# Performance work log

Hardware: AMD Instinct MI355X
Metric: run time of the kernel (lower is better)

## Reference

```python
import jax, jax.numpy as jnp
import numpy as np

DIM = 3            # point feature dim (xyz)
POS_HID = 64       # pos_mlp hidden
ATTN_HID = DIM * 4 # attn_mlp hidden (mult=4)
N_NBR = 16         # points per group
GROUPS = 512       # groups per batch element
MLP_D = N_NBR * DIM  # 48


def setup_inputs() -> dict:
    key = jax.random.key(0)
    ks = jax.random.split(key, 20)
    B = 32
    s = lambda *sh: 1.0 / np.sqrt(sh[0])
    inp = {
        "original_points": jax.random.normal(ks[0], (B, GROUPS, DIM), jnp.float32),
        "data": jax.random.normal(ks[1], (B, GROUPS, N_NBR, DIM), jnp.float32),
        # PointTransformerLayer params
        "w_qkv": jax.random.normal(ks[2], (DIM, DIM * 3), jnp.float32) * s(DIM),
        "pos_w1": jax.random.normal(ks[3], (3, POS_HID), jnp.float32) * s(3),
        "pos_b1": jnp.zeros((POS_HID,), jnp.float32),
        "pos_w2": jax.random.normal(ks[4], (POS_HID, DIM), jnp.float32) * s(POS_HID),
        "pos_b2": jnp.zeros((DIM,), jnp.float32),
        "attn_w1": jax.random.normal(ks[5], (DIM, ATTN_HID), jnp.float32) * s(DIM),
        "attn_b1": jnp.zeros((ATTN_HID,), jnp.float32),
        "attn_w2": jax.random.normal(ks[6], (ATTN_HID, DIM), jnp.float32) * s(ATTN_HID),
        "attn_b2": jnp.zeros((DIM,), jnp.float32),
        # downstream MLP params
        "mlp_w1": jax.random.normal(ks[7], (MLP_D, MLP_D), jnp.float32) * s(MLP_D),
        "mlp_b1": jnp.zeros((MLP_D,), jnp.float32),
        "mlp_w2": jax.random.normal(ks[8], (MLP_D, MLP_D), jnp.float32) * s(MLP_D),
        "mlp_b2": jnp.zeros((MLP_D,), jnp.float32),
        "mlp_w3": jax.random.normal(ks[9], (MLP_D, 1), jnp.float32) * s(MLP_D),
        "mlp_b3": jnp.zeros((1,), jnp.float32),
    }
    return inp


def reference(original_points, data, w_qkv, pos_w1, pos_b1, pos_w2, pos_b2,
              attn_w1, attn_b1, attn_w2, attn_b2,
              mlp_w1, mlp_b1, mlp_w2, mlp_b2, mlp_w3, mlp_b3):
    B, G, n, d = data.shape
    x = data.reshape(B * G, n, d)          # (BG, n, 3)
    pos = x[:, :, :3]                       # pos == features here (f=3)

    # Point-transformer vector attention
    qkv = x @ w_qkv                          # (BG, n, 9)
    q, k, v = jnp.split(qkv, 3, axis=-1)
    rel_pos = pos[:, :, None, :] - pos[:, None, :, :]              # (BG, n, n, 3)
    rel_emb = jax.nn.relu(rel_pos @ pos_w1 + pos_b1) @ pos_w2 + pos_b2  # (BG, n, n, 3)
    qk_rel = q[:, :, None, :] - k[:, None, :, :]                   # (BG, n, n, 3)
    v_ij = v[:, None, :, :] + rel_emb                              # (BG, n, n, 3)
    sim = jax.nn.relu((qk_rel + rel_emb) @ attn_w1 + attn_b1) @ attn_w2 + attn_b2
    attn = jax.nn.softmax(sim, axis=-2)                            # softmax over j
    agg = jnp.einsum('bijd,bijd->bid', attn, v_ij)                 # (BG, n, 3)

    # regroup into (B, 512, 48) exactly as stack(split(512, dim=0))
    sa = agg.reshape(B, G, n * d)
    h = jax.nn.relu(sa @ mlp_w1 + mlp_b1)
    h = jax.nn.relu(h @ mlp_w2 + mlp_b2)
    return h @ mlp_w3 + mlp_b3              # (B, 512, 1)
```

## Files before the change

kernel.cpp:

```cpp
#include <hip/hip_runtime.h>


typedef _Float16 h2 __attribute__((ext_vector_type(2)));
typedef _Float16 h8 __attribute__((ext_vector_type(8)));

#define AH_STRIDE 36
#define WP_STRIDE 36

union H8U { h8 v; h2 p[4]; unsigned u[4]; };

__device__ __forceinline__ h2 pkrtz(float a, float b) {
    return __builtin_bit_cast(h2, __builtin_amdgcn_cvt_pkrtz(a, b));
}

#if __has_builtin(__builtin_amdgcn_fdot2)
__device__ __forceinline__ float dot2acc(h2 a, h2 b, float c) {
    return __builtin_amdgcn_fdot2(a, b, c, false);
}
#else
__device__ __forceinline__ float dot2acc(h2 a, h2 b, float c) {
    return fmaf((float)a.x, (float)b.x, fmaf((float)a.y, (float)b.y, c));
}
#endif

__device__ __forceinline__ float dpp_add16(float x) {
    float s = x;
    int t;
    t = __builtin_amdgcn_update_dpp(0, __builtin_bit_cast(int, s), 0x121, 0xf, 0xf, false);
    s += __builtin_bit_cast(float, t);
    t = __builtin_amdgcn_update_dpp(0, __builtin_bit_cast(int, s), 0x122, 0xf, 0xf, false);
    s += __builtin_bit_cast(float, t);
    t = __builtin_amdgcn_update_dpp(0, __builtin_bit_cast(int, s), 0x124, 0xf, 0xf, false);
    s += __builtin_bit_cast(float, t);
    t = __builtin_amdgcn_update_dpp(0, __builtin_bit_cast(int, s), 0x128, 0xf, 0xf, false);
    s += __builtin_bit_cast(float, t);
    return s;
}

__global__ __launch_bounds__(256) void pt_main(
    const float* __restrict__ data,
    const float* __restrict__ wqkv,
    const float* __restrict__ pw1,
    const float* __restrict__ pb1,
    const float* __restrict__ pw2,
    const float* __restrict__ pb2,
    const float* __restrict__ aw1,
    const float* __restrict__ ab1,
    const float* __restrict__ aw2,
    const float* __restrict__ ab2,
    const float* __restrict__ mw1,
    const float* __restrict__ mb1,
    const float* __restrict__ mw2,
    const float* __restrict__ mb2,
    const float* __restrict__ mw3,
    const float* __restrict__ mb3,
    float* __restrict__ out)
{
    __shared__ __attribute__((aligned(16))) float s_pos[48];
    __shared__ __attribute__((aligned(16))) float s_q[48], s_k[48], s_v[48];
    __shared__ __attribute__((aligned(16))) float s_sa[48], s_h1[48];
    __shared__ __attribute__((aligned(16))) unsigned s_a1h[16 * AH_STRIDE];
    __shared__ __attribute__((aligned(16))) unsigned s_a2h[16 * AH_STRIDE];
    __shared__ __attribute__((aligned(16))) unsigned s_wp[3 * WP_STRIDE];

    const int g = blockIdx.x;
    const int t = threadIdx.x;

    if (t < 48) s_pos[t] = data[g * 48 + t];
    __syncthreads();

    if (t < 48) {
        const int sec = t >> 4, p = t & 15;
        const float x0 = s_pos[p*3+0], x1 = s_pos[p*3+1], x2 = s_pos[p*3+2];
        float* dst = (sec == 0) ? s_q : (sec == 1) ? s_k : s_v;
        #pragma unroll
        for (int c = 0; c < 3; ++c) {
            dst[p*3+c] = fmaf(x0, wqkv[0*9 + sec*3 + c],
                         fmaf(x1, wqkv[1*9 + sec*3 + c],
                         x2 * wqkv[2*9 + sec*3 + c]));
        }
    }

    {
        const int ii = t >> 4;
        const int hc = (t & 15) << 2;
        const float x0 = s_pos[ii*3+0], x1 = s_pos[ii*3+1], x2 = s_pos[ii*3+2];
        float s[4];
        #pragma unroll
        for (int c = 0; c < 4; ++c) {
            const int h = hc + c;
            s[c] = fmaf(x0, pw1[h], fmaf(x1, pw1[64+h], x2 * pw1[128+h]));
        }
        h2 a1p0 = pkrtz(s[0] + pb1[hc+0], s[1] + pb1[hc+1]);
        h2 a1p1 = pkrtz(s[2] + pb1[hc+2], s[3] + pb1[hc+3]);
        h2 a2p0 = pkrtz(s[0], s[1]);
        h2 a2p1 = pkrtz(s[2], s[3]);
        const int base = ii * AH_STRIDE + (hc >> 1);
        s_a1h[base+0] = __builtin_bit_cast(unsigned, a1p0);
        s_a1h[base+1] = __builtin_bit_cast(unsigned, a1p1);
        s_a2h[base+0] = __builtin_bit_cast(unsigned, a2p0);
        s_a2h[base+1] = __builtin_bit_cast(unsigned, a2p1);
    }

    if (t < 96) {
        const int hp = t & 31, c = t >> 5;
        h2 wpair = pkrtz(pw2[(2*hp)*3 + c], pw2[(2*hp+1)*3 + c]);
        s_wp[c * WP_STRIDE + hp] = __builtin_bit_cast(unsigned, wpair);
    }
    __syncthreads();

    const int i = t >> 4, j = t & 15;

    float e0 = pb2[0], e1 = pb2[1], e2 = pb2[2];
    #pragma unroll
    for (int cc = 0; cc < 8; ++cc) {
        H8U ai, aj, w0, w1, w2;
        ai.v = *(const h8*)&s_a1h[i * AH_STRIDE + cc*4];
        aj.v = *(const h8*)&s_a2h[j * AH_STRIDE + cc*4];
        w0.v = *(const h8*)&s_wp[0 * WP_STRIDE + cc*4];
        w1.v = *(const h8*)&s_wp[1 * WP_STRIDE + cc*4];
        w2.v = *(const h8*)&s_wp[2 * WP_STRIDE + cc*4];
        #pragma unroll
        for (int m = 0; m < 4; ++m) {
            h2 d = ai.p[m] - aj.p[m];
            h2 z = {(_Float16)0, (_Float16)0};
            h2 r = { d.x > z.x ? d.x : z.x, d.y > z.y ? d.y : z.y };
            e0 = dot2acc(r, w0.p[m], e0);
            e1 = dot2acc(r, w1.p[m], e1);
            e2 = dot2acc(r, w2.p[m], e2);
        }
    }

    const float vi0 = s_v[j*3+0] + e0, vi1 = s_v[j*3+1] + e1, vi2 = s_v[j*3+2] + e2;
    const float si0 = s_q[i*3+0] - s_k[j*3+0] + e0;
    const float si1 = s_q[i*3+1] - s_k[j*3+1] + e1;
    const float si2 = s_q[i*3+2] - s_k[j*3+2] + e2;

    float m0 = ab2[0], m1 = ab2[1], m2 = ab2[2];
    #pragma unroll
    for (int gg = 0; gg < 12; ++gg) {
        float hg = fmaf(si0, aw1[gg], fmaf(si1, aw1[12+gg], fmaf(si2, aw1[24+gg], ab1[gg])));
        hg = fmaxf(hg, 0.0f);
        m0 = fmaf(hg, aw2[gg*3+0], m0);
        m1 = fmaf(hg, aw2[gg*3+1], m1);
        m2 = fmaf(hg, aw2[gg*3+2], m2);
    }

    const float L2E = 1.44269504f;
    const float p0 = __builtin_amdgcn_exp2f(m0 * L2E);
    const float p1 = __builtin_amdgcn_exp2f(m1 * L2E);
    const float p2 = __builtin_amdgcn_exp2f(m2 * L2E);

    const float n0 = dpp_add16(p0 * vi0);
    const float n1 = dpp_add16(p1 * vi1);
    const float n2 = dpp_add16(p2 * vi2);
    const float d0 = dpp_add16(p0);
    const float d1 = dpp_add16(p1);
    const float d2 = dpp_add16(p2);

    if (j == 0) {
        s_sa[i*3+0] = n0 * __builtin_amdgcn_rcpf(d0);
        s_sa[i*3+1] = n1 * __builtin_amdgcn_rcpf(d1);
        s_sa[i*3+2] = n2 * __builtin_amdgcn_rcpf(d2);
    }
    __syncthreads();

    if (t < 48) {
        float h1 = mb1[t];
        #pragma unroll
        for (int c = 0; c < 48; ++c) h1 = fmaf(s_sa[c], mw1[c*48+t], h1);
        s_h1[t] = fmaxf(h1, 0.0f);
    }
    __syncthreads();

    float fv = 0.0f;
    if (t < 48) {
        float h2v = mb2[t];
        #pragma unroll
        for (int c = 0; c < 48; ++c) h2v = fmaf(s_h1[c], mw2[c*48+t], h2v);
        h2v = fmaxf(h2v, 0.0f);
        fv = h2v * mw3[t];
    }
    if (t < 64) {
        #pragma unroll
        for (int mk = 1; mk < 64; mk <<= 1) fv += __shfl_xor(fv, mk);
        if (t == 0) out[g] = fv + mb3[0];
    }
}

extern "C" void kernel_launch(void* const* d_in, const int* in_sizes, int n_in,
                              void* d_out, int out_size, void* d_ws, size_t ws_size,
                              hipStream_t stream) {
    const float* data = (const float*)d_in[1];
    const int groups = out_size;

    pt_main<<<groups, 256, 0, stream>>>(
        data,
        (const float*)d_in[2],  (const float*)d_in[3],  (const float*)d_in[4],
        (const float*)d_in[5],  (const float*)d_in[6],  (const float*)d_in[7],
        (const float*)d_in[8],  (const float*)d_in[9],  (const float*)d_in[10],
        (const float*)d_in[11], (const float*)d_in[12], (const float*)d_in[13],
        (const float*)d_in[14], (const float*)d_in[15], (const float*)d_in[16],
        (float*)d_out);
}
```

Before: 143.6 us.

## Prepack fp16 weights in a pre-kernel and run attention MLP in packed half

Adds a tiny pre-kernel that packs the pos_mlp second-layer and attn_mlp weights and biases into fp16 pairs in the workspace. The main kernel then reads them as uniform (scalar) loads instead of building them in shared memory per block. The attn_mlp hidden layer is recomputed with packed half FMAs and dot2 accumulation. q/k/v are stored padded to float4 so each needs a single vector LDS load. This adds a second launch and lowers precision in the attention MLP, which risks accuracy.

```diff
diff --git a/kernel.cpp b/kernel.cpp
--- a/kernel.cpp
+++ b/kernel.cpp
@@ -5,12 +5,14 @@
 typedef _Float16 h8 __attribute__((ext_vector_type(8)));
 
 #define AH_STRIDE 36
-#define WP_STRIDE 36
 
 union H8U { h8 v; h2 p[4]; unsigned u[4]; };
 
 __device__ __forceinline__ h2 pkrtz(float a, float b) {
     return __builtin_bit_cast(h2, __builtin_amdgcn_cvt_pkrtz(a, b));
+}
+__device__ __forceinline__ h2 uash2(unsigned u) {
+    return __builtin_bit_cast(h2, u);
 }
 
 #if __has_builtin(__builtin_amdgcn_fdot2)
@@ -35,6 +37,25 @@
     t = __builtin_amdgcn_update_dpp(0, __builtin_bit_cast(int, s), 0x128, 0xf, 0xf, false);
     s += __builtin_bit_cast(float, t);
     return s;
+}
+
+__global__ void wpack(const float* __restrict__ pw2, const float* __restrict__ aw1,
+                      const float* __restrict__ ab1, const float* __restrict__ aw2,
+                      unsigned* __restrict__ ws) {
+    const int t = threadIdx.x;
+    if (t < 96) {
+        const int hp = t & 31, c = t >> 5;
+        ws[c*32+hp] = __builtin_bit_cast(unsigned, pkrtz(pw2[(2*hp)*3+c], pw2[(2*hp+1)*3+c]));
+    } else if (t < 114) {
+        const int idx = t - 96, r = idx / 6, gp = idx % 6;
+        ws[96+r*6+gp] = __builtin_bit_cast(unsigned, pkrtz(aw1[r*12+2*gp], aw1[r*12+2*gp+1]));
+    } else if (t < 120) {
+        const int gp = t - 114;
+        ws[114+gp] = __builtin_bit_cast(unsigned, pkrtz(ab1[2*gp], ab1[2*gp+1]));
+    } else if (t < 138) {
+        const int idx = t - 120, gp = idx / 3, c = idx % 3;
+        ws[120+gp*3+c] = __builtin_bit_cast(unsigned, pkrtz(aw2[(2*gp)*3+c], aw2[(2*gp+1)*3+c]));
+    }
 }
 
 __global__ __launch_bounds__(256) void pt_main(
@@ -42,11 +63,7 @@
     const float* __restrict__ wqkv,
     const float* __restrict__ pw1,
     const float* __restrict__ pb1,
-    const float* __restrict__ pw2,
     const float* __restrict__ pb2,
-    const float* __restrict__ aw1,
-    const float* __restrict__ ab1,
-    const float* __restrict__ aw2,
     const float* __restrict__ ab2,
     const float* __restrict__ mw1,
     const float* __restrict__ mb1,
@@ -54,14 +71,14 @@
     const float* __restrict__ mb2,
     const float* __restrict__ mw3,
     const float* __restrict__ mb3,
+    const unsigned* __restrict__ wsp,
     float* __restrict__ out)
 {
     __shared__ __attribute__((aligned(16))) float s_pos[48];
-    __shared__ __attribute__((aligned(16))) float s_q[48], s_k[48], s_v[48];
+    __shared__ __attribute__((aligned(16))) float s_q4[64], s_k4[64], s_v4[64];
     __shared__ __attribute__((aligned(16))) float s_sa[48], s_h1[48];
     __shared__ __attribute__((aligned(16))) unsigned s_a1h[16 * AH_STRIDE];
     __shared__ __attribute__((aligned(16))) unsigned s_a2h[16 * AH_STRIDE];
-    __shared__ __attribute__((aligned(16))) unsigned s_wp[3 * WP_STRIDE];
 
     const int g = blockIdx.x;
     const int t = threadIdx.x;
@@ -72,13 +89,14 @@
     if (t < 48) {
         const int sec = t >> 4, p = t & 15;
         const float x0 = s_pos[p*3+0], x1 = s_pos[p*3+1], x2 = s_pos[p*3+2];
-        float* dst = (sec == 0) ? s_q : (sec == 1) ? s_k : s_v;
+        float* dst = (sec == 0) ? s_q4 : (sec == 1) ? s_k4 : s_v4;
         #pragma unroll
         for (int c = 0; c < 3; ++c) {
-            dst[p*3+c] = fmaf(x0, wqkv[0*9 + sec*3 + c],
+            dst[p*4+c] = fmaf(x0, wqkv[0*9 + sec*3 + c],
                          fmaf(x1, wqkv[1*9 + sec*3 + c],
                          x2 * wqkv[2*9 + sec*3 + c]));
         }
+        dst[p*4+3] = 0.0f;
     }
 
     {
@@ -101,12 +119,6 @@
         s_a2h[base+0] = __builtin_bit_cast(unsigned, a2p0);
         s_a2h[base+1] = __builtin_bit_cast(unsigned, a2p1);
     }
-
-    if (t < 96) {
-        const int hp = t & 31, c = t >> 5;
-        h2 wpair = pkrtz(pw2[(2*hp)*3 + c], pw2[(2*hp+1)*3 + c]);
-        s_wp[c * WP_STRIDE + hp] = __builtin_bit_cast(unsigned, wpair);
-    }
     __syncthreads();
 
     const int i = t >> 4, j = t & 15;
@@ -114,36 +126,42 @@
     float e0 = pb2[0], e1 = pb2[1], e2 = pb2[2];
     #pragma unroll
     for (int cc = 0; cc < 8; ++cc) {
-        H8U ai, aj, w0, w1, w2;
+        H8U ai, aj;
         ai.v = *(const h8*)&s_a1h[i * AH_STRIDE + cc*4];
         aj.v = *(const h8*)&s_a2h[j * AH_STRIDE + cc*4];
-        w0.v = *(const h8*)&s_wp[0 * WP_STRIDE + cc*4];
-        w1.v = *(const h8*)&s_wp[1 * WP_STRIDE + cc*4];
-        w2.v = *(const h8*)&s_wp[2 * WP_STRIDE + cc*4];
         #pragma unroll
         for (int m = 0; m < 4; ++m) {
+            const int hp = cc*4 + m;
             h2 d = ai.p[m] - aj.p[m];
             h2 z = {(_Float16)0, (_Float16)0};
             h2 r = { d.x > z.x ? d.x : z.x, d.y > z.y ? d.y : z.y };
-            e0 = dot2acc(r, w0.p[m], e0);
-            e1 = dot2acc(r, w1.p[m], e1);
-            e2 = dot2acc(r, w2.p[m], e2);
+            e0 = dot2acc(r, uash2(wsp[0*32+hp]), e0);
+            e1 = dot2acc(r, uash2(wsp[1*32+hp]), e1);
+            e2 = dot2acc(r, uash2(wsp[2*32+hp]), e2);
         }
     }
 
-    const float vi0 = s_v[j*3+0] + e0, vi1 = s_v[j*3+1] + e1, vi2 = s_v[j*3+2] + e2;
-    const float si0 = s_q[i*3+0] - s_k[j*3+0] + e0;
-    const float si1 = s_q[i*3+1] - s_k[j*3+1] + e1;
-    const float si2 = s_q[i*3+2] - s_k[j*3+2] + e2;
-
+    const float4 qv = *(const float4*)&s_q4[i*4];
+    const float4 kv = *(const float4*)&s_k4[j*4];
+    const float4 vv = *(const float4*)&s_v4[j*4];
+    const float vi0 = vv.x + e0, vi1 = vv.y + e1, vi2 = vv.z + e2;
+    const float si0 = qv.x - kv.x + e0;
+    const float si1 = qv.y - kv.y + e1;
+    const float si2 = qv.z - kv.z + e2;
+
+    const h2 sx = pkrtz(si0, si0), sy = pkrtz(si1, si1), sz = pkrtz(si2, si2);
+    const h2 z2 = {(_Float16)0, (_Float16)0};
     float m0 = ab2[0], m1 = ab2[1], m2 = ab2[2];
     #pragma unroll
-    for (int gg = 0; gg < 12; ++gg) {
-        float hg = fmaf(si0, aw1[gg], fmaf(si1, aw1[12+gg], fmaf(si2, aw1[24+gg], ab1[gg])));
-        hg = fmaxf(hg, 0.0f);
-        m0 = fmaf(hg, aw2[gg*3+0], m0);
-        m1 = fmaf(hg, aw2[gg*3+1], m1);
-        m2 = fmaf(hg, aw2[gg*3+2], m2);
+    for (int gp = 0; gp < 6; ++gp) {
+        h2 acc = uash2(wsp[114+gp]);
+        acc = __builtin_elementwise_fma(sx, uash2(wsp[96+0*6+gp]), acc);
+        acc = __builtin_elementwise_fma(sy, uash2(wsp[96+1*6+gp]), acc);
+        acc = __builtin_elementwise_fma(sz, uash2(wsp[96+2*6+gp]), acc);
+        h2 hg = { acc.x > z2.x ? acc.x : z2.x, acc.y > z2.y ? acc.y : z2.y };
+        m0 = dot2acc(hg, uash2(wsp[120+gp*3+0]), m0);
+        m1 = dot2acc(hg, uash2(wsp[120+gp*3+1]), m1);
+        m2 = dot2acc(hg, uash2(wsp[120+gp*3+2]), m2);
     }
 
     const float L2E = 1.44269504f;
@@ -192,14 +210,29 @@
                               void* d_out, int out_size, void* d_ws, size_t ws_size,
                               hipStream_t stream) {
     const float* data = (const float*)d_in[1];
+    unsigned* ws = (unsigned*)d_ws;
     const int groups = out_size;
+
+    wpack<<<1, 256, 0, stream>>>(
+        (const float*)d_in[5],
+        (const float*)d_in[7],
+        (const float*)d_in[8],
+        (const float*)d_in[9],
+        ws);
 
     pt_main<<<groups, 256, 0, stream>>>(
         data,
-        (const float*)d_in[2],  (const float*)d_in[3],  (const float*)d_in[4],
-        (const float*)d_in[5],  (const float*)d_in[6],  (const float*)d_in[7],
-        (const float*)d_in[8],  (const float*)d_in[9],  (const float*)d_in[10],
-        (const float*)d_in[11], (const float*)d_in[12], (const float*)d_in[13],
-        (const float*)d_in[14], (const float*)d_in[15], (const float*)d_in[16],
+        (const float*)d_in[2],
+        (const float*)d_in[3],
+        (const float*)d_in[4],
+        (const float*)d_in[6],
+        (const float*)d_in[10],
+        (const float*)d_in[11],
+        (const float*)d_in[12],
+        (const float*)d_in[13],
+        (const float*)d_in[14],
+        (const float*)d_in[15],
+        (const float*)d_in[16],
+        ws,
         (float*)d_out);
 }
```

Result: faster. 139.3 us (-3.0%).
